# Kernel optimization log

Hardware: AMD Instinct MI355X
Metric: run time of the kernel (lower is better)

Reference implementation:

```python
import jax, jax.numpy as jnp
import numpy as np

ACT_BITS = 8
W_BITS = 8
BN_EPS = 1e-5


def _round_ste(x):
    # straight-through round (HAWQ-style ste_round)
    return x + jax.lax.stop_gradient(jnp.round(x) - x)


def _quant_sym(x, bits):
    # symmetric per-tensor fake quantization; scale treated as constant (EMA min/max in original)
    n = float(2 ** (bits - 1) - 1)
    s = jax.lax.stop_gradient(jnp.maximum(jnp.max(jnp.abs(x)) / n, 1e-8))
    xq = jnp.clip(_round_ste(x / s), -n - 1.0, n) * s
    return xq, s


def _conv(x, w, stride, pad):
    return jax.lax.conv_general_dilated(
        x, w, (stride, stride), [(pad, pad), (pad, pad)],
        dimension_numbers=("NCHW", "OIHW", "NCHW"))


def _quant_bn(x, gamma, beta, mean, var):
    # fold BN into a per-channel scale+bias; quantize the folded scale like a weight
    ws = gamma * jax.lax.rsqrt(var + BN_EPS)          # [C]
    wq, ws_scale = _quant_sym(ws, W_BITS)
    b = beta - mean * wq                               # [C]
    return x * wq[None, :, None, None] + b[None, :, None, None], ws_scale


def setup_inputs() -> dict:
    key = jax.random.key(0)
    ks = jax.random.split(key, 16)
    d = {}
    d["x"] = jax.random.normal(ks[0], (32, 128, 56, 56), jnp.float32)
    d["w1"] = jax.random.normal(ks[1], (256, 128, 3, 3), jnp.float32) * 0.05
    d["w2"] = jax.random.normal(ks[2], (256, 256, 3, 3), jnp.float32) * 0.05
    d["w_id"] = jax.random.normal(ks[3], (256, 128, 1, 1), jnp.float32) * 0.05
    for i, pfx in enumerate(["bn1", "bn2", "id"]):
        k4 = jax.random.split(ks[4 + i], 4)
        d[pfx + "_gamma"] = jax.random.uniform(k4[0], (256,), jnp.float32) + 0.5
        d[pfx + "_beta"] = jax.random.normal(k4[1], (256,), jnp.float32) * 0.1
        d[pfx + "_mean"] = jax.random.normal(k4[2], (256,), jnp.float32) * 0.1
        d[pfx + "_var"] = jax.random.uniform(k4[3], (256,), jnp.float32) + 0.5
    return d


def reference(x, w1, w2, w_id,
              bn1_gamma, bn1_beta, bn1_mean, bn1_var,
              bn2_gamma, bn2_beta, bn2_mean, bn2_var,
              id_gamma, id_beta, id_mean, id_var):
    # quant_act on block input
    xq, act_s = _quant_sym(x, ACT_BITS)

    # identity branch: 1x1 stride-2 quantized conv -> quant_act -> folded quant bn
    w_id_q, _ = _quant_sym(w_id, W_BITS)
    identity = _conv(xq, w_id_q, 2, 0)
    identity, _ = _quant_sym(identity, ACT_BITS)
    identity, _ = _quant_bn(identity, id_gamma, id_beta, id_mean, id_var)

    # main branch conv1 (3x3 stride 2) -> act quant -> bn -> relu -> act quant
    w1_q, _ = _quant_sym(w1, W_BITS)
    h = _conv(xq, w1_q, 2, 1)
    h, _ = _quant_sym(h, ACT_BITS)
    h, _ = _quant_bn(h, bn1_gamma, bn1_beta, bn1_mean, bn1_var)
    h = jax.nn.relu(h)
    h, _ = _quant_sym(h, ACT_BITS)

    # conv2 (3x3 stride 1) -> act quant -> bn
    w2_q, _ = _quant_sym(w2, W_BITS)
    h = _conv(h, w2_q, 1, 1)
    h, _ = _quant_sym(h, ACT_BITS)
    h, _ = _quant_bn(h, bn2_gamma, bn2_beta, bn2_mean, bn2_var)

    # residual add -> int32 requant -> relu
    h = h + identity
    h, out_s = _quant_sym(h, ACT_BITS)
    h = jax.nn.relu(h)
    return h, out_s
```

## Files before the change

kernel.cpp:

```cpp
#include <hip/hip_runtime.h>
#include <limits.h>

#define THREADS 256
#define GRID_BLOCKS 896

typedef int vi4 __attribute__((ext_vector_type(4)));

__device__ __forceinline__ float clamp8f(float q) { return fminf(fmaxf(q, -128.0f), 127.0f); }
__device__ __forceinline__ float sc_from_bits(unsigned b) {
  return fmaxf(__uint_as_float(b) / 127.0f, 1e-8f);
}
__device__ __forceinline__ signed char q8(float v, float s) {
  return (signed char)(int)clamp8f(rintf(v / s));
}


__device__ __forceinline__ void gbar(int* IS, int base, int bx) {
  asm volatile("s_waitcnt vmcnt(0)" ::: "memory");
  int old = __hip_atomic_fetch_add(IS + base + (bx & 7) * 16, 1, __ATOMIC_RELAXED,
                                   __HIP_MEMORY_SCOPE_AGENT);
  if (old == 111) {
    int r = __hip_atomic_fetch_add(IS + base + 128, 1, __ATOMIC_RELAXED, __HIP_MEMORY_SCOPE_AGENT);
    if (r == 7)
      __hip_atomic_fetch_add(IS + base + 144, 1, __ATOMIC_RELAXED, __HIP_MEMORY_SCOPE_AGENT);
  }
  while (__hip_atomic_load(IS + base + 144, __ATOMIC_RELAXED, __HIP_MEMORY_SCOPE_SYSTEM) == 0)
    __builtin_amdgcn_s_sleep(2);
}

__device__ __forceinline__ void amax_body(const float4* __restrict__ p, int n4, int bid,
                                          int nblocks, int* __restrict__ slot) {
  const int tid = threadIdx.x;
  const int stride = nblocks * THREADS;
  float m = 0.0f;
  int i = bid * THREADS + tid;
  for (; i + 3 * stride < n4; i += 4 * stride) {
    float4 v0 = p[i];
    float4 v1 = p[i + stride];
    float4 v2 = p[i + 2 * stride];
    float4 v3 = p[i + 3 * stride];
    float m0 = fmaxf(fmaxf(fabsf(v0.x), fabsf(v0.y)), fmaxf(fabsf(v0.z), fabsf(v0.w)));
    float m1 = fmaxf(fmaxf(fabsf(v1.x), fabsf(v1.y)), fmaxf(fabsf(v1.z), fabsf(v1.w)));
    float m2 = fmaxf(fmaxf(fabsf(v2.x), fabsf(v2.y)), fmaxf(fabsf(v2.z), fabsf(v2.w)));
    float m3 = fmaxf(fmaxf(fabsf(v3.x), fabsf(v3.y)), fmaxf(fabsf(v3.z), fabsf(v3.w)));
    m = fmaxf(m, fmaxf(fmaxf(m0, m1), fmaxf(m2, m3)));
  }
  for (; i < n4; i += stride) {
    float4 v = p[i];
    m = fmaxf(m, fmaxf(fmaxf(fabsf(v.x), fabsf(v.y)), fmaxf(fabsf(v.z), fabsf(v.w))));
  }
#pragma unroll
  for (int k = 32; k >= 1; k >>= 1) m = fmaxf(m, __shfl_xor(m, k));
  __shared__ float wred[4];
  if ((tid & 63) == 0) wred[tid >> 6] = m;
  __syncthreads();
  if (tid == 0) {
    m = fmaxf(fmaxf(wred[0], wred[1]), fmaxf(wred[2], wred[3]));
    atomicMax(slot, __float_as_int(m));
  }
}

__global__ __launch_bounds__(THREADS) void k_pre(
    int* IS, const float* g1, const float* be1, const float* m1, const float* v1, float* wq1,
    float* b1, const float* g2, const float* be2, const float* m2, const float* v2, float* wq2,
    float* b2, const float* gi, const float* bei, const float* mi, const float* vvi, float* wqi,
    float* bi, const float4* w1, const float4* w2, const float4* wid, const float4* x) {
  int b = blockIdx.x;
  int c = threadIdx.x;
  if (b < 3) {
    if (b == 0) {
      IS[128 + c] = 0;
      IS[384 + c] = 0;
      IS[640 + c] = 0;
      if (c < 32) IS[896 + c] = 0;
    }
    const float *gamma, *beta, *mean, *var;
    float *wq, *bb;
    if (b == 0) { gamma = g1; beta = be1; mean = m1; var = v1; wq = wq1; bb = b1; }
    else if (b == 1) { gamma = g2; beta = be2; mean = m2; var = v2; wq = wq2; bb = b2; }
    else { gamma = gi; beta = bei; mean = mi; var = vvi; wq = wqi; bb = bi; }
    __shared__ float red[THREADS];
    float ws = gamma[c] * (1.0f / sqrtf(var[c] + 1e-5f));
    red[c] = fabsf(ws);
    __syncthreads();
    for (int s = THREADS / 2; s > 0; s >>= 1) {
      if (c < s) red[c] = fmaxf(red[c], red[c + s]);
      __syncthreads();
    }
    float sws = fmaxf(red[0] / 127.0f, 1e-8f);
    float q = clamp8f(rintf(ws / sws)) * sws;
    wq[c] = q;
    bb[c] = beta[c] - mean[c] * q;
    return;
  }
  b -= 3;
  if (b < 64) { amax_body(w1, 73728, b, 64, IS + 1); return; }
  b -= 64;
  if (b < 128) { amax_body(w2, 147456, b, 128, IS + 2); return; }
  b -= 128;
  if (b < 16) { amax_body(wid, 8192, b, 16, IS + 3); return; }
  b -= 16;
  amax_body(x, 3211264, b, 512, IS + 0);
}

__global__ __launch_bounds__(THREADS) void k_quant(const float* __restrict__ x,
                                                   int* __restrict__ X8,
                                                   const float* __restrict__ w1f,
                                                   vi4* __restrict__ W1m,
                                                   const float* __restrict__ w2f,
                                                   vi4* __restrict__ W2m,
                                                   const float* __restrict__ widf,
                                                   vi4* __restrict__ Widm,
                                                   const unsigned* __restrict__ ISu) {
  __shared__ signed char tile[56 * 132];
  int b = blockIdx.x;
  int t = threadIdx.x;
  if (b < 1792) {
    float s = sc_from_bits(ISu[0]);
    int h = b % 56, n = b / 56;
    const float* xp = x + ((n * 128) * 56 + h) * 56;
#pragma unroll
    for (int k = 0; k < 28; ++k) {
      int i = t + k * 256;
      int w = i % 56, c = i / 56;
      tile[w * 132 + c] = q8(xp[c * 3136 + w], s);
    }
    __syncthreads();
    int* op = X8 + (n * 56 + h) * 56 * 32;
#pragma unroll
    for (int k = 0; k < 7; ++k) {
      int i = t + k * 256;
      int w = i >> 5, c4 = (i & 31) * 4;
      const signed char* tp = tile + w * 132 + c4;
      op[i] = (int)(unsigned char)tp[0] | ((int)(unsigned char)tp[1] << 8) |
              ((int)(unsigned char)tp[2] << 16) | ((int)(unsigned char)tp[3] << 24);
    }
    return;
  }
  if (b < 1864) {
    int tt = (b - 1792) * THREADS + t;
    float s = sc_from_bits(ISu[1]);
    int lane = tt & 63;
    int cotile = (tt >> 6) & 15;
    int ks = tt >> 10;
    int tap = ks >> 1, kc = ks & 1;
    int kh = tap / 3, kw = tap % 3;
    int co = cotile * 16 + (lane & 15);
    int ci0 = kc * 64 + (lane >> 4) * 16;
    const float* src = w1f + (co * 128 + ci0) * 9 + kh * 3 + kw;
    int r[4];
#pragma unroll
    for (int q = 0; q < 4; ++q) {
      unsigned b0 = (unsigned char)q8(src[(q * 4 + 0) * 9], s);
      unsigned b1 = (unsigned char)q8(src[(q * 4 + 1) * 9], s);
      unsigned b2 = (unsigned char)q8(src[(q * 4 + 2) * 9], s);
      unsigned b3 = (unsigned char)q8(src[(q * 4 + 3) * 9], s);
      r[q] = (int)(b0 | (b1 << 8) | (b2 << 16) | (b3 << 24));
    }
    vi4 v = {r[0], r[1], r[2], r[3]};
    W1m[tt] = v;
    return;
  }
  if (b < 2008) {
    int tt = (b - 1864) * THREADS + t;
    float s = sc_from_bits(ISu[2]);
    int lane = tt & 63;
    int cotile = (tt >> 6) & 15;
    int ks = tt >> 10;
    int tap = ks >> 2, kc = ks & 3;
    int kh = tap / 3, kw = tap % 3;
    int co = cotile * 16 + (lane & 15);
    int ci0 = kc * 64 + (lane >> 4) * 16;
    const float* src = w2f + (co * 256 + ci0) * 9 + kh * 3 + kw;
    int r[4];
#pragma unroll
    for (int q = 0; q < 4; ++q) {
      unsigned b0 = (unsigned char)q8(src[(q * 4 + 0) * 9], s);
      unsigned b1 = (unsigned char)q8(src[(q * 4 + 1) * 9], s);
      unsigned b2 = (unsigned char)q8(src[(q * 4 + 2) * 9], s);
      unsigned b3 = (unsigned char)q8(src[(q * 4 + 3) * 9], s);
      r[q] = (int)(b0 | (b1 << 8) | (b2 << 16) | (b3 << 24));
    }
    vi4 v = {r[0], r[1], r[2], r[3]};
    W2m[tt] = v;
    return;
  }
  {
    int tt = (b - 2008) * THREADS + t;
    float s = sc_from_bits(ISu[3]);
    int lane = tt & 63;
    int cotile = (tt >> 6) & 15;
    int ks = tt >> 10;
    int co = cotile * 16 + (lane & 15);
    int ci0 = ks * 64 + (lane >> 4) * 16;
    const float* src = widf + co * 128 + ci0;
    int r[4];
#pragma unroll
    for (int q = 0; q < 4; ++q) {
      unsigned b0 = (unsigned char)q8(src[q * 4 + 0], s);
      unsigned b1 = (unsigned char)q8(src[q * 4 + 1], s);
      unsigned b2 = (unsigned char)q8(src[q * 4 + 2], s);
      unsigned b3 = (unsigned char)q8(src[q * 4 + 3], s);
      r[q] = (int)(b0 | (b1 << 8) | (b2 << 16) | (b3 << 24));
    }
    vi4 v = {r[0], r[1], r[2], r[3]};
    Widm[tt] = v;
  }
}

#define MFMA_I8(a, b, c) __builtin_amdgcn_mfma_i32_16x16x64_i8(a, b, c, 0, 0, 0)

__device__ __forceinline__ signed char qact(int v, float sxw, float s_h1, float s_y2, float wq,
                                            float bb) {
  float hf = (float)v * sxw;
  float q = clamp8f(rintf(hf / s_h1));
  float hv = q * s_h1;
  float y = fmaxf(hv * wq + bb, 0.0f);
  float a = fminf(fmaxf(rintf(y / s_y2), -128.0f), 127.0f);
  return (signed char)(int)a;
}

__global__ __launch_bounds__(THREADS, 4) void k_cv1(const int* X8, const vi4* __restrict__ W1m,
                                                    const vi4* __restrict__ Widm,
                                                    int* __restrict__ IDI, int* A2i, int* IS,
                                                    const float* __restrict__ wq1,
                                                    const float* __restrict__ b1, float* SC,
                                                    int* maxS2, int* minS2) {
  __shared__ __align__(16) int lds[9280];
  __shared__ int redA[4];
  __shared__ int sVmax, sVmin;
  __shared__ float sSxw, sSh1, sSy2;
  const int tid = threadIdx.x;
  const int bx = blockIdx.x;
  const int n = bx / 28, rr = bx % 28;
  const int hp = rr >> 1, nh = rr & 1;
  const int ho0 = hp * 2;
  vi4 zero = {0, 0, 0, 0};

  for (int r = 0; r < 5; ++r) {
    int h = 2 * ho0 - 1 + r;
    int* dst = lds + r * 58 * 32;
    if (h >= 0 && h < 56) {
      const vi4* src = (const vi4*)(X8 + (n * 56 + h) * 56 * 32);
      for (int i4 = tid; i4 < 448; i4 += THREADS) {
        int col = i4 >> 3, e0 = (i4 & 7) * 4;
        int cell = r * 58 + col + 1;
        *(vi4*)(lds + cell * 32 + (e0 ^ ((cell & 7) << 2))) = src[i4];
      }
      if (tid < 32) dst[tid] = 0;
      else if (tid >= 128 && tid < 160) dst[57 * 32 + (tid - 128)] = 0;
    } else {
      for (int i4 = tid; i4 < 464; i4 += THREADS) ((vi4*)dst)[i4] = zero;
    }
  }
  __syncthreads();

  const int lane = tid & 63, wv = tid >> 6;
  const int mw = wv & 1, nw = wv >> 1;
  const int lm = lane & 15, quad = lane >> 4;
  const int woc0 = lm, woc1 = (16 + lm) > 27 ? 27 : (16 + lm);
  const int choff = quad * 4;
  const int ho = ho0 + mw;
  const int obase = ((n * 28 + ho) * 28) * 256;
  const int ctbase = nh * 8 + nw * 4;

#define LDA(row, colp, sub)                                                              \
  (*(const vi4*)(lds + ((row) * 58 + (colp)) * 32 +                                      \
                 ((sub) ^ ((((row) * 58 + (colp)) & 7) << 2))))

  vi4 acc[2][4];
  vi4 bA[4], bB[4];
  vi4 a0A, a1A, a0B, a1B;

#pragma unroll
  for (int mt = 0; mt < 2; ++mt)
#pragma unroll
    for (int ct = 0; ct < 4; ++ct) acc[mt][ct] = zero;
  const vi4* wibase = Widm + ctbase * 64 + lane;
  {
    const int row = 2 * mw + 1;
#pragma unroll
    for (int kc = 0; kc < 2; ++kc) {
      vi4 a0 = LDA(row, 2 * woc0 + 1, kc * 16 + choff);
      vi4 a1 = LDA(row, 2 * woc1 + 1, kc * 16 + choff);
#pragma unroll
      for (int ct = 0; ct < 4; ++ct) {
        vi4 b = wibase[kc * 1024 + ct * 64];
        acc[0][ct] = MFMA_I8(a0, b, acc[0][ct]);
        acc[1][ct] = MFMA_I8(a1, b, acc[1][ct]);
      }
    }
  }
  int am = 0;
#pragma unroll
  for (int ct = 0; ct < 4; ++ct) {
    const int co = (ctbase + ct) * 16 + lm;
#pragma unroll
    for (int mt = 0; mt < 2; ++mt)
#pragma unroll
      for (int r = 0; r < 4; ++r) {
        int wo = mt * 16 + quad * 4 + r;
        if (wo < 28) {
          int v = acc[mt][ct][r];
          IDI[obase + wo * 256 + co] = v;
          am = max(am, v < 0 ? -v : v);
        }
      }
  }
#pragma unroll
  for (int k = 32; k >= 1; k >>= 1) am = max(am, __shfl_xor(am, k));
  if (lane == 0) redA[wv] = am;

#pragma unroll
  for (int mt = 0; mt < 2; ++mt)
#pragma unroll
    for (int ct = 0; ct < 4; ++ct) acc[mt][ct] = zero;
  const vi4* wbase = W1m + ctbase * 64 + lane;
#pragma unroll
  for (int ct = 0; ct < 4; ++ct) bA[ct] = wbase[ct * 64];
  {
    a0A = LDA(2 * mw, 2 * woc0, choff);
    a1A = LDA(2 * mw, 2 * woc1, choff);
  }
#pragma unroll 1
  for (int ks = 0; ks < 18; ks += 2) {
    {
      const int ksn = ks + 1;
      const int khn = (ksn >= 6) + (ksn >= 12);
      const int t2 = ksn - khn * 6;
      const int kwn = t2 >> 1, kcn = t2 & 1;
#pragma unroll
      for (int ct = 0; ct < 4; ++ct) bB[ct] = wbase[ksn * 1024 + ct * 64];
      const int row = 2 * mw + khn;
      a0B = LDA(row, 2 * woc0 + kwn, kcn * 16 + choff);
      a1B = LDA(row, 2 * woc1 + kwn, kcn * 16 + choff);
    }
#pragma unroll
    for (int ct = 0; ct < 4; ++ct) {
      acc[0][ct] = MFMA_I8(a0A, bA[ct], acc[0][ct]);
      acc[1][ct] = MFMA_I8(a1A, bA[ct], acc[1][ct]);
    }
    if (ks + 2 < 18) {
      const int ksn = ks + 2;
      const int khn = (ksn >= 6) + (ksn >= 12);
      const int t2 = ksn - khn * 6;
      const int kwn = t2 >> 1, kcn = t2 & 1;
#pragma unroll
      for (int ct = 0; ct < 4; ++ct) bA[ct] = wbase[ksn * 1024 + ct * 64];
      const int row = 2 * mw + khn;
      a0A = LDA(row, 2 * woc0 + kwn, kcn * 16 + choff);
      a1A = LDA(row, 2 * woc1 + kwn, kcn * 16 + choff);
    }
#pragma unroll
    for (int ct = 0; ct < 4; ++ct) {
      acc[0][ct] = MFMA_I8(a0B, bB[ct], acc[0][ct]);
      acc[1][ct] = MFMA_I8(a1B, bB[ct], acc[1][ct]);
    }
  }

#pragma unroll
  for (int ct = 0; ct < 4; ++ct) {
    int vmax = INT_MIN, vmin = INT_MAX;
#pragma unroll
    for (int mt = 0; mt < 2; ++mt)
#pragma unroll
      for (int r = 0; r < 4; ++r) {
        int wo = mt * 16 + quad * 4 + r;
        if (wo < 28) {
          int v = acc[mt][ct][r];
          vmax = max(vmax, v);
          vmin = min(vmin, v);
        }
      }
    vmax = max(vmax, __shfl_xor(vmax, 16));
    vmax = max(vmax, __shfl_xor(vmax, 32));
    vmin = min(vmin, __shfl_xor(vmin, 16));
    vmin = min(vmin, __shfl_xor(vmin, 32));
    if (lane < 16) {
      int cl = (nw * 4 + ct) * 16 + lane;
      __hip_atomic_store(maxS2 + bx * 256 + mw * 128 + cl, vmax, __ATOMIC_RELAXED,
                         __HIP_MEMORY_SCOPE_AGENT);
      __hip_atomic_store(minS2 + bx * 256 + mw * 128 + cl, vmin, __ATOMIC_RELAXED,
                         __HIP_MEMORY_SCOPE_AGENT);
    }
  }

  __syncthreads();
  if (tid == 0) {
    int a = max(max(redA[0], redA[1]), max(redA[2], redA[3]));
    atomicMax(IS + 5, a);
  }
#pragma unroll
  for (int ct = 0; ct < 4; ++ct) {
    const int cl = (nw * 4 + ct) * 16 + lm;
#pragma unroll
    for (int mt = 0; mt < 2; ++mt)
#pragma unroll
      for (int r = 0; r < 4; ++r) {
        int wo = mt * 16 + quad * 4 + r;
        if (wo < 28) lds[(mw * 28 + wo) * 130 + cl] = acc[mt][ct][r];
      }
  }
  __syncthreads();
  if (tid == 0) gbar(IS, 128, bx);
  __syncthreads();

  if (bx < 256) {
    const int c = bx, nhc = c >> 7, cl = c & 127;
    int vmax = INT_MIN, vmin = INT_MAX;
    for (int j = tid; j < 896; j += THREADS) {
      int bxx = nhc + ((j >> 1) << 1);
      int mwj = j & 1;
      int a = __hip_atomic_load(maxS2 + bxx * 256 + mwj * 128 + cl, __ATOMIC_RELAXED,
                                __HIP_MEMORY_SCOPE_AGENT);
      int i_ = __hip_atomic_load(minS2 + bxx * 256 + mwj * 128 + cl, __ATOMIC_RELAXED,
                                 __HIP_MEMORY_SCOPE_AGENT);
      vmax = max(vmax, a);
      vmin = min(vmin, i_);
    }
    int* rMax = lds + 7280;
    int* rMin = lds + 7536;
    rMax[tid] = vmax;
    rMin[tid] = vmin;
    __syncthreads();
    for (int s = 128; s > 0; s >>= 1) {
      if (tid < s) {
        rMax[tid] = max(rMax[tid], rMax[tid + s]);
        rMin[tid] = min(rMin[tid], rMin[tid + s]);
      }
      __syncthreads();
    }
    if (tid == 0) {
      sVmax = rMax[0];
      sVmin = rMin[0];
      int a1 = sVmax < 0 ? -sVmax : sVmax;
      int a0 = sVmin < 0 ? -sVmin : sVmin;
      atomicMax(IS + 4, max(a1, a0));
    }
  }
  __syncthreads();
  if (tid == 0) gbar(IS, 288, bx);
  __syncthreads();

  if (bx < 256 && tid == 0) {
    float sx = sc_from_bits((unsigned)__hip_atomic_load(IS + 0, __ATOMIC_RELAXED,
                                                        __HIP_MEMORY_SCOPE_AGENT));
    float sw1 = sc_from_bits((unsigned)__hip_atomic_load(IS + 1, __ATOMIC_RELAXED,
                                                         __HIP_MEMORY_SCOPE_AGENT));
    int mh1 = __hip_atomic_load(IS + 4, __ATOMIC_RELAXED, __HIP_MEMORY_SCOPE_AGENT);
    float sxw = sx * sw1;
    float s_h1 = fmaxf(sxw * (float)mh1 / 127.0f, 1e-8f);
    float wq = wq1[bx], bbc = b1[bx];
    float q1 = clamp8f(rintf((float)sVmax * sxw / s_h1));
    float q0 = clamp8f(rintf((float)sVmin * sxw / s_h1));
    float y1 = fmaxf(q1 * s_h1 * wq + bbc, 0.0f);
    float y0 = fmaxf(q0 * s_h1 * wq + bbc, 0.0f);
    atomicMax(IS + 7, __float_as_int(fmaxf(y1, y0)));
  }
  __syncthreads();
  if (tid == 0) gbar(IS, 448, bx);
  __syncthreads();

  if (tid == 0) {
    float sx = sc_from_bits((unsigned)__hip_atomic_load(IS + 0, __ATOMIC_RELAXED,
                                                        __HIP_MEMORY_SCOPE_AGENT));
    float sw1 = sc_from_bits((unsigned)__hip_atomic_load(IS + 1, __ATOMIC_RELAXED,
                                                         __HIP_MEMORY_SCOPE_AGENT));
    int mh1 = __hip_atomic_load(IS + 4, __ATOMIC_RELAXED, __HIP_MEMORY_SCOPE_AGENT);
    int mrf = __hip_atomic_load(IS + 7, __ATOMIC_RELAXED, __HIP_MEMORY_SCOPE_AGENT);
    float sxw = sx * sw1;
    float s_h1 = fmaxf(sxw * (float)mh1 / 127.0f, 1e-8f);
    float s_y2 = fmaxf(__int_as_float(mrf) / 127.0f, 1e-8f);
    sSxw = sxw;
    sSh1 = s_h1;
    sSy2 = s_y2;
    if (bx == 0) {
      int mid = __hip_atomic_load(IS + 5, __ATOMIC_RELAXED, __HIP_MEMORY_SCOPE_AGENT);
      float swid = sc_from_bits((unsigned)__hip_atomic_load(IS + 3, __ATOMIC_RELAXED,
                                                            __HIP_MEMORY_SCOPE_AGENT));
      SC[9] = s_y2;
      SC[10] = fmaxf(sx * swid * (float)mid / 127.0f, 1e-8f);
    }
  }
  __syncthreads();

  {
    const float sxw = sSxw, s_h1 = sSh1, s_y2 = sSy2;
#pragma unroll
    for (int k = 0; k < 7; ++k) {
      int i = tid + k * 256;
      int sp = i >> 5, c4i = i & 31;
      int mwp = sp >= 28 ? 1 : 0;
      int wo = sp - mwp * 28;
      int c0 = nh * 128 + c4i * 4;
      const int* pk = lds + sp * 130 + c4i * 4;
      unsigned r0 = (unsigned char)qact(pk[0], sxw, s_h1, s_y2, wq1[c0], b1[c0]);
      unsigned r1 = (unsigned char)qact(pk[1], sxw, s_h1, s_y2, wq1[c0 + 1], b1[c0 + 1]);
      unsigned r2 = (unsigned char)qact(pk[2], sxw, s_h1, s_y2, wq1[c0 + 2], b1[c0 + 2]);
      unsigned r3 = (unsigned char)qact(pk[3], sxw, s_h1, s_y2, wq1[c0 + 3], b1[c0 + 3]);
      A2i[((n * 28 + ho0 + mwp) * 28 + wo) * 64 + nh * 32 + c4i] =
          (int)(r0 | (r1 << 8) | (r2 << 16) | (r3 << 24));
    }
  }
#undef LDA
}

struct SumParams {
  float sxw2, s_h2, sxwid, s_idq;
};
__device__ __forceinline__ float sum_val(int v2, int vi, const SumParams& P, float wq2c, float b2c,
                                         float wqidc, float bidc) {
  float q2 = clamp8f(rintf((float)v2 * P.sxw2 / P.s_h2));
  float z = (q2 * P.s_h2) * wq2c + b2c;
  float qi = clamp8f(rintf((float)vi * P.sxwid / P.s_idq));
  float zi = (qi * P.s_idq) * wqidc + bidc;
  return z + zi;
}
__device__ __forceinline__ SumParams make_params2(const float* SC, const unsigned* ISu, int mh2) {
  SumParams P;
  float sx = sc_from_bits(ISu[0]);
  float sw2 = sc_from_bits(ISu[2]);
  float swid = sc_from_bits(ISu[3]);
  float s_y2 = SC[9];
  P.s_idq = SC[10];
  P.sxw2 = s_y2 * sw2;
  P.s_h2 = fmaxf(P.sxw2 * (float)mh2 / 127.0f, 1e-8f);
  P.sxwid = sx * swid;
  return P;
}

__global__ __launch_bounds__(THREADS, 4) void k_tail(const int* __restrict__ A2,
                                                     const vi4* __restrict__ W2m,
                                                     const int* __restrict__ IDI,
                                                     const float* SC, int* IS,
                                                     const float* __restrict__ wq2,
                                                     const float* __restrict__ b2,
                                                     const float* __restrict__ wqid,
                                                     const float* __restrict__ bidp,
                                                     float* __restrict__ out) {
  __shared__ __align__(16) int lds[4 * 30 * 68];
  __shared__ int redA[4];
  __shared__ float redF[4];
  __shared__ int sMh2;
  __shared__ float sOutS;
  const int tid = threadIdx.x;
  const int bx = blockIdx.x;
  const int n = bx / 28, rr = bx % 28;
  const int hp = rr >> 1, nh = rr & 1;
  const int ho0 = hp * 2;
  vi4 zero = {0, 0, 0, 0};

  for (int r = 0; r < 4; ++r) {
    int h = ho0 - 1 + r;
    int* dst = lds + r * 30 * 68;
    if (h >= 0 && h < 28) {
      const vi4* src = (const vi4*)(A2 + (n * 28 + h) * 28 * 64);
      for (int i4 = tid; i4 < 448; i4 += THREADS) {
        int col = i4 >> 4, c = (i4 & 15) * 4;
        *(vi4*)(dst + (col + 1) * 68 + c) = src[i4];
      }
      if (tid < 64) dst[tid] = 0;
      else if (tid >= 128 && tid < 192) dst[29 * 68 + (tid - 128)] = 0;
    } else {
      for (int i4 = tid; i4 < 510; i4 += THREADS) ((vi4*)dst)[i4] = zero;
    }
  }
  __syncthreads();

  const int lane = tid & 63, wv = tid >> 6;
  const int mw = wv & 1, nw = wv >> 1;
  const int lm = lane & 15, quad = lane >> 4;
  const int woc0 = lm, woc1 = (16 + lm) > 27 ? 27 : (16 + lm);
  const int choff = quad * 4;
  const int ctbase = nh * 8 + nw * 4;

  vi4 acc[2][4];
  vi4 bA[4], bB[4];
  vi4 a0A, a1A, a0B, a1B;
#pragma unroll
  for (int mt = 0; mt < 2; ++mt)
#pragma unroll
    for (int ct = 0; ct < 4; ++ct) acc[mt][ct] = zero;

  const vi4* wbase = W2m + ctbase * 64 + lane;
#pragma unroll
  for (int ct = 0; ct < 4; ++ct) bA[ct] = wbase[ct * 64];
  {
    const int ro = mw * 30;
    a0A = *(const vi4*)(lds + (ro + woc0) * 68 + choff);
    a1A = *(const vi4*)(lds + (ro + woc1) * 68 + choff);
  }
#pragma unroll 1
  for (int ks = 0; ks < 36; ks += 2) {
    {
      const int ksn = ks + 1;
      const int khn = (ksn >= 12) + (ksn >= 24);
      const int t2 = ksn - khn * 12;
      const int kwn = t2 >> 2, kcn = t2 & 3;
#pragma unroll
      for (int ct = 0; ct < 4; ++ct) bB[ct] = wbase[ksn * 1024 + ct * 64];
      const int ro = (mw + khn) * 30;
      a0B = *(const vi4*)(lds + (ro + woc0 + kwn) * 68 + kcn * 16 + choff);
      a1B = *(const vi4*)(lds + (ro + woc1 + kwn) * 68 + kcn * 16 + choff);
    }
#pragma unroll
    for (int ct = 0; ct < 4; ++ct) {
      acc[0][ct] = MFMA_I8(a0A, bA[ct], acc[0][ct]);
      acc[1][ct] = MFMA_I8(a1A, bA[ct], acc[1][ct]);
    }
    if (ks + 2 < 36) {
      const int ksn = ks + 2;
      const int khn = (ksn >= 12) + (ksn >= 24);
      const int t2 = ksn - khn * 12;
      const int kwn = t2 >> 2, kcn = t2 & 3;
#pragma unroll
      for (int ct = 0; ct < 4; ++ct) bA[ct] = wbase[ksn * 1024 + ct * 64];
      const int ro = (mw + khn) * 30;
      a0A = *(const vi4*)(lds + (ro + woc0 + kwn) * 68 + kcn * 16 + choff);
      a1A = *(const vi4*)(lds + (ro + woc1 + kwn) * 68 + kcn * 16 + choff);
    }
#pragma unroll
    for (int ct = 0; ct < 4; ++ct) {
      acc[0][ct] = MFMA_I8(a0B, bB[ct], acc[0][ct]);
      acc[1][ct] = MFMA_I8(a1B, bB[ct], acc[1][ct]);
    }
  }

  int am = 0;
#pragma unroll
  for (int ct = 0; ct < 4; ++ct)
#pragma unroll
    for (int mt = 0; mt < 2; ++mt)
#pragma unroll
      for (int r = 0; r < 4; ++r) {
        int wo = mt * 16 + quad * 4 + r;
        if (wo < 28) {
          int v = acc[mt][ct][r];
          am = max(am, v < 0 ? -v : v);
        }
      }
#pragma unroll
  for (int k = 32; k >= 1; k >>= 1) am = max(am, __shfl_xor(am, k));
  if (lane == 0) redA[wv] = am;
  __syncthreads();
  if (tid == 0) {
    int a = max(max(redA[0], redA[1]), max(redA[2], redA[3]));
    atomicMax(IS + 6, a);
  }

  int* sumsi = lds;
  float* sums = (float*)lds;
  const int ib = ((n * 28 + ho0) * 28) * 256 + nh * 128;
#pragma unroll
  for (int k = 0; k < 28; ++k) {
    int idx = tid + k * 256;
    int cl = idx & 127, sp = idx >> 7;
    sumsi[cl * 57 + sp] = IDI[ib + sp * 256 + cl];
  }
  __syncthreads();
  if (tid == 0) {
    gbar(IS, 608, bx);
    sMh2 = __hip_atomic_load(IS + 6, __ATOMIC_RELAXED, __HIP_MEMORY_SCOPE_SYSTEM);
  }
  __syncthreads();
  const SumParams P = make_params2(SC, (const unsigned*)IS, sMh2);

  float fm = 0.0f;
#pragma unroll
  for (int ct = 0; ct < 4; ++ct) {
    const int co = (ctbase + ct) * 16 + lm;
    const int cl = co - nh * 128;
    float w2c = wq2[co], b2c = b2[co], wic = wqid[co], bic = bidp[co];
#pragma unroll
    for (int mt = 0; mt < 2; ++mt)
#pragma unroll
      for (int r = 0; r < 4; ++r) {
        int wo = mt * 16 + quad * 4 + r;
        if (wo < 28) {
          int slot = cl * 57 + mw * 28 + wo;
          float sv = sum_val(acc[mt][ct][r], sumsi[slot], P, w2c, b2c, wic, bic);
          sums[slot] = sv;
          fm = fmaxf(fm, fabsf(sv));
        }
      }
  }
#pragma unroll
  for (int k = 32; k >= 1; k >>= 1) fm = fmaxf(fm, __shfl_xor(fm, k));
  if (lane == 0) redF[wv] = fm;
  __syncthreads();
  if (tid == 0) {
    float a = fmaxf(fmaxf(redF[0], redF[1]), fmaxf(redF[2], redF[3]));
    atomicMax(IS + 11, __float_as_int(a));
    gbar(IS, 768, bx);
    int mb = __hip_atomic_load(IS + 11, __ATOMIC_RELAXED, __HIP_MEMORY_SCOPE_SYSTEM);
    sOutS = fmaxf(__int_as_float(mb) / 127.0f, 1e-8f);
  }
  __syncthreads();
  const float out_s = sOutS;

  float* ob = out + n * 200704 + (nh * 128) * 784 + ho0 * 28;
#pragma unroll
  for (int k = 0; k < 28; ++k) {
    int idx = tid + k * 256;
    int cl = idx / 56, rem = idx % 56;
    float sv = sums[cl * 57 + rem];
    float q = clamp8f(rintf(sv / out_s));
    ob[cl * 784 + rem] = q > 0.0f ? q * out_s : 0.0f;
  }
  if (bx == 0 && tid == 0) out[6422528] = out_s;
}

extern "C" void kernel_launch(void* const* d_in, const int* in_sizes, int n_in, void* d_out,
                              int out_size, void* d_ws, size_t ws_size, hipStream_t stream) {
  (void)in_sizes; (void)n_in; (void)out_size; (void)ws_size;
  const float* x = (const float*)d_in[0];
  const float* w1 = (const float*)d_in[1];
  const float* w2 = (const float*)d_in[2];
  const float* wid = (const float*)d_in[3];
  const float* bn1g = (const float*)d_in[4];
  const float* bn1b = (const float*)d_in[5];
  const float* bn1m = (const float*)d_in[6];
  const float* bn1v = (const float*)d_in[7];
  const float* bn2g = (const float*)d_in[8];
  const float* bn2b = (const float*)d_in[9];
  const float* bn2m = (const float*)d_in[10];
  const float* bn2v = (const float*)d_in[11];
  const float* idg = (const float*)d_in[12];
  const float* idb = (const float*)d_in[13];
  const float* idm = (const float*)d_in[14];
  const float* idv = (const float*)d_in[15];

  char* ws = (char*)d_ws;
  float* SC = (float*)ws;
  int* IS = (int*)ws;
  unsigned* ISu = (unsigned*)ws;
  float* wq1 = (float*)(ws + 4096);
  float* b1 = (float*)(ws + 5120);
  float* wq2 = (float*)(ws + 6144);
  float* b2 = (float*)(ws + 7168);
  float* wqid = (float*)(ws + 8192);
  float* bid = (float*)(ws + 9216);
  char* X8 = ws + 16384;
  char* A2 = X8;
  char* W1m = X8 + 12845056;
  char* W2m = W1m + 294912;
  char* Widm = W2m + 589824;
  int* IDI = (int*)(Widm + 32768);
  float* out = (float*)d_out;
  int* maxS2 = (int*)d_out;
  int* minS2 = maxS2 + 896 * 256;

  k_pre<<<723, THREADS, 0, stream>>>(IS, bn1g, bn1b, bn1m, bn1v, wq1, b1, bn2g, bn2b, bn2m, bn2v,
                                     wq2, b2, idg, idb, idm, idv, wqid, bid, (const float4*)w1,
                                     (const float4*)w2, (const float4*)wid, (const float4*)x);
  k_quant<<<2016, THREADS, 0, stream>>>(x, (int*)X8, w1, (vi4*)W1m, w2, (vi4*)W2m, wid,
                                        (vi4*)Widm, ISu);
  k_cv1<<<GRID_BLOCKS, THREADS, 0, stream>>>((const int*)X8, (const vi4*)W1m, (const vi4*)Widm,
                                             IDI, (int*)A2, IS, wq1, b1, SC, maxS2, minS2);
  k_tail<<<GRID_BLOCKS, THREADS, 0, stream>>>((const int*)A2, (const vi4*)W2m, (const int*)IDI, SC,
                                              IS, wq2, b2, wqid, bid, out);
}
```

Before: 246.9 us.

## Fuse prep and quant kernels via grid barrier; drop cv1 per-channel exchange phase

Merges the BN-fold/amax kernel and the int8 quantization kernel into one 2016-block kernel. The two phases are separated by a software grid barrier, and launch bounds request 8 blocks per CU so every block can be resident at once. In the conv1 kernel, the cross-block per-channel min/max exchange and its extra grid barrier are removed: each block computes the post-BN/ReLU max from its own per-channel extrema and contributes it with an atomicMax. Barrier counters are now cleared with a hipMemsetAsync instead of inside the prep kernel. This saves a kernel launch and a global synchronization round. The cost is that correctness depends on all 2016 blocks being co-resident, which risks a deadlock if register or LDS use limits occupancy.

```diff
diff --git a/kernel.cpp b/kernel.cpp
--- a/kernel.cpp
+++ b/kernel.cpp
@@ -15,11 +15,11 @@
 }
 
 
-__device__ __forceinline__ void gbar(int* IS, int base, int bx) {
+__device__ __forceinline__ void gbar(int* IS, int base, int bx, int subTgt) {
   asm volatile("s_waitcnt vmcnt(0)" ::: "memory");
   int old = __hip_atomic_fetch_add(IS + base + (bx & 7) * 16, 1, __ATOMIC_RELAXED,
                                    __HIP_MEMORY_SCOPE_AGENT);
-  if (old == 111) {
+  if (old == subTgt - 1) {
     int r = __hip_atomic_fetch_add(IS + base + 128, 1, __ATOMIC_RELAXED, __HIP_MEMORY_SCOPE_AGENT);
     if (r == 7)
       __hip_atomic_fetch_add(IS + base + 144, 1, __ATOMIC_RELAXED, __HIP_MEMORY_SCOPE_AGENT);
@@ -60,63 +60,66 @@
   }
 }
 
-__global__ __launch_bounds__(THREADS) void k_pre(
+__device__ __forceinline__ float sc_slot(const int* IS, int slot) {
+  unsigned u = (unsigned)__hip_atomic_load((int*)(IS + slot), __ATOMIC_RELAXED,
+                                           __HIP_MEMORY_SCOPE_AGENT);
+  return fmaxf(__uint_as_float(u) / 127.0f, 1e-8f);
+}
+
+__global__ __launch_bounds__(THREADS, 8) void k_pq(
     int* IS, const float* g1, const float* be1, const float* m1, const float* v1, float* wq1,
     float* b1, const float* g2, const float* be2, const float* m2, const float* v2, float* wq2,
     float* b2, const float* gi, const float* bei, const float* mi, const float* vvi, float* wqi,
-    float* bi, const float4* w1, const float4* w2, const float4* wid, const float4* x) {
-  int b = blockIdx.x;
-  int c = threadIdx.x;
-  if (b < 3) {
-    if (b == 0) {
-      IS[128 + c] = 0;
-      IS[384 + c] = 0;
-      IS[640 + c] = 0;
-      if (c < 32) IS[896 + c] = 0;
-    }
-    const float *gamma, *beta, *mean, *var;
-    float *wq, *bb;
-    if (b == 0) { gamma = g1; beta = be1; mean = m1; var = v1; wq = wq1; bb = b1; }
-    else if (b == 1) { gamma = g2; beta = be2; mean = m2; var = v2; wq = wq2; bb = b2; }
-    else { gamma = gi; beta = bei; mean = mi; var = vvi; wq = wqi; bb = bi; }
-    __shared__ float red[THREADS];
-    float ws = gamma[c] * (1.0f / sqrtf(var[c] + 1e-5f));
-    red[c] = fabsf(ws);
-    __syncthreads();
-    for (int s = THREADS / 2; s > 0; s >>= 1) {
-      if (c < s) red[c] = fmaxf(red[c], red[c + s]);
+    float* bi, const float* x, int* X8, const float* w1f, vi4* W1m, const float* w2f, vi4* W2m,
+    const float* widf, vi4* Widm) {
+  __shared__ signed char tile[56 * 132];
+  __shared__ float red[THREADS];
+  const int bx = blockIdx.x;
+  const int t = threadIdx.x;
+
+  {
+    int b = bx;
+    if (b < 3) {
+      const float *gamma, *beta, *mean, *var;
+      float *wq, *bb;
+      if (b == 0) { gamma = g1; beta = be1; mean = m1; var = v1; wq = wq1; bb = b1; }
+      else if (b == 1) { gamma = g2; beta = be2; mean = m2; var = v2; wq = wq2; bb = b2; }
+      else { gamma = gi; beta = bei; mean = mi; var = vvi; wq = wqi; bb = bi; }
+      int c = t;
+      float ws = gamma[c] * (1.0f / sqrtf(var[c] + 1e-5f));
+      red[c] = fabsf(ws);
       __syncthreads();
-    }
-    float sws = fmaxf(red[0] / 127.0f, 1e-8f);
-    float q = clamp8f(rintf(ws / sws)) * sws;
-    wq[c] = q;
-    bb[c] = beta[c] - mean[c] * q;
-    return;
-  }
-  b -= 3;
-  if (b < 64) { amax_body(w1, 73728, b, 64, IS + 1); return; }
-  b -= 64;
-  if (b < 128) { amax_body(w2, 147456, b, 128, IS + 2); return; }
-  b -= 128;
-  if (b < 16) { amax_body(wid, 8192, b, 16, IS + 3); return; }
-  b -= 16;
-  amax_body(x, 3211264, b, 512, IS + 0);
-}
-
-__global__ __launch_bounds__(THREADS) void k_quant(const float* __restrict__ x,
-                                                   int* __restrict__ X8,
-                                                   const float* __restrict__ w1f,
-                                                   vi4* __restrict__ W1m,
-                                                   const float* __restrict__ w2f,
-                                                   vi4* __restrict__ W2m,
-                                                   const float* __restrict__ widf,
-                                                   vi4* __restrict__ Widm,
-                                                   const unsigned* __restrict__ ISu) {
-  __shared__ signed char tile[56 * 132];
-  int b = blockIdx.x;
-  int t = threadIdx.x;
+      for (int s = THREADS / 2; s > 0; s >>= 1) {
+        if (c < s) red[c] = fmaxf(red[c], red[c + s]);
+        __syncthreads();
+      }
+      float sws = fmaxf(red[0] / 127.0f, 1e-8f);
+      float q = clamp8f(rintf(ws / sws)) * sws;
+      wq[c] = q;
+      bb[c] = beta[c] - mean[c] * q;
+    } else {
+      b -= 3;
+      if (b < 64) {
+        amax_body((const float4*)w1f, 73728, b, 64, IS + 1);
+      } else {
+        b -= 64;
+        if (b < 128) {
+          amax_body((const float4*)w2f, 147456, b, 128, IS + 2);
+        } else {
+          b -= 128;
+          if (b < 16) amax_body((const float4*)widf, 8192, b, 16, IS + 3);
+          else amax_body((const float4*)x, 3211264, b - 16, 1805, IS + 0);
+        }
+      }
+    }
+  }
+  __syncthreads();
+  if (t == 0) gbar(IS, 128, bx, 252);
+  __syncthreads();
+
+  int b = bx;
   if (b < 1792) {
-    float s = sc_from_bits(ISu[0]);
+    float s = sc_slot(IS, 0);
     int h = b % 56, n = b / 56;
     const float* xp = x + ((n * 128) * 56 + h) * 56;
 #pragma unroll
@@ -139,7 +142,7 @@
   }
   if (b < 1864) {
     int tt = (b - 1792) * THREADS + t;
-    float s = sc_from_bits(ISu[1]);
+    float s = sc_slot(IS, 1);
     int lane = tt & 63;
     int cotile = (tt >> 6) & 15;
     int ks = tt >> 10;
@@ -152,10 +155,10 @@
 #pragma unroll
     for (int q = 0; q < 4; ++q) {
       unsigned b0 = (unsigned char)q8(src[(q * 4 + 0) * 9], s);
-      unsigned b1 = (unsigned char)q8(src[(q * 4 + 1) * 9], s);
-      unsigned b2 = (unsigned char)q8(src[(q * 4 + 2) * 9], s);
+      unsigned b1v = (unsigned char)q8(src[(q * 4 + 1) * 9], s);
+      unsigned b2v = (unsigned char)q8(src[(q * 4 + 2) * 9], s);
       unsigned b3 = (unsigned char)q8(src[(q * 4 + 3) * 9], s);
-      r[q] = (int)(b0 | (b1 << 8) | (b2 << 16) | (b3 << 24));
+      r[q] = (int)(b0 | (b1v << 8) | (b2v << 16) | (b3 << 24));
     }
     vi4 v = {r[0], r[1], r[2], r[3]};
     W1m[tt] = v;
@@ -163,7 +166,7 @@
   }
   if (b < 2008) {
     int tt = (b - 1864) * THREADS + t;
-    float s = sc_from_bits(ISu[2]);
+    float s = sc_slot(IS, 2);
     int lane = tt & 63;
     int cotile = (tt >> 6) & 15;
     int ks = tt >> 10;
@@ -176,10 +179,10 @@
 #pragma unroll
     for (int q = 0; q < 4; ++q) {
       unsigned b0 = (unsigned char)q8(src[(q * 4 + 0) * 9], s);
-      unsigned b1 = (unsigned char)q8(src[(q * 4 + 1) * 9], s);
-      unsigned b2 = (unsigned char)q8(src[(q * 4 + 2) * 9], s);
+      unsigned b1v = (unsigned char)q8(src[(q * 4 + 1) * 9], s);
+      unsigned b2v = (unsigned char)q8(src[(q * 4 + 2) * 9], s);
       unsigned b3 = (unsigned char)q8(src[(q * 4 + 3) * 9], s);
-      r[q] = (int)(b0 | (b1 << 8) | (b2 << 16) | (b3 << 24));
+      r[q] = (int)(b0 | (b1v << 8) | (b2v << 16) | (b3 << 24));
     }
     vi4 v = {r[0], r[1], r[2], r[3]};
     W2m[tt] = v;
@@ -187,7 +190,7 @@
   }
   {
     int tt = (b - 2008) * THREADS + t;
-    float s = sc_from_bits(ISu[3]);
+    float s = sc_slot(IS, 3);
     int lane = tt & 63;
     int cotile = (tt >> 6) & 15;
     int ks = tt >> 10;
@@ -198,10 +201,10 @@
 #pragma unroll
     for (int q = 0; q < 4; ++q) {
       unsigned b0 = (unsigned char)q8(src[q * 4 + 0], s);
-      unsigned b1 = (unsigned char)q8(src[q * 4 + 1], s);
-      unsigned b2 = (unsigned char)q8(src[q * 4 + 2], s);
+      unsigned b1v = (unsigned char)q8(src[q * 4 + 1], s);
+      unsigned b2v = (unsigned char)q8(src[q * 4 + 2], s);
       unsigned b3 = (unsigned char)q8(src[q * 4 + 3], s);
-      r[q] = (int)(b0 | (b1 << 8) | (b2 << 16) | (b3 << 24));
+      r[q] = (int)(b0 | (b1v << 8) | (b2v << 16) | (b3 << 24));
     }
     vi4 v = {r[0], r[1], r[2], r[3]};
     Widm[tt] = v;
@@ -224,11 +227,10 @@
                                                     const vi4* __restrict__ Widm,
                                                     int* __restrict__ IDI, int* A2i, int* IS,
                                                     const float* __restrict__ wq1,
-                                                    const float* __restrict__ b1, float* SC,
-                                                    int* maxS2, int* minS2) {
+                                                    const float* __restrict__ b1, float* SC) {
   __shared__ __align__(16) int lds[9280];
-  __shared__ int redA[4];
-  __shared__ int sVmax, sVmin;
+  __shared__ int redA[4], redB[4];
+  __shared__ float redF[4];
   __shared__ float sSxw, sSh1, sSy2;
   const int tid = threadIdx.x;
   const int bx = blockIdx.x;
@@ -358,6 +360,8 @@
     }
   }
 
+  int vmx[4], vmn[4];
+  int am1 = 0;
 #pragma unroll
   for (int ct = 0; ct < 4; ++ct) {
     int vmax = INT_MIN, vmin = INT_MAX;
@@ -376,20 +380,15 @@
     vmax = max(vmax, __shfl_xor(vmax, 32));
     vmin = min(vmin, __shfl_xor(vmin, 16));
     vmin = min(vmin, __shfl_xor(vmin, 32));
-    if (lane < 16) {
-      int cl = (nw * 4 + ct) * 16 + lane;
-      __hip_atomic_store(maxS2 + bx * 256 + mw * 128 + cl, vmax, __ATOMIC_RELAXED,
-                         __HIP_MEMORY_SCOPE_AGENT);
-      __hip_atomic_store(minS2 + bx * 256 + mw * 128 + cl, vmin, __ATOMIC_RELAXED,
-                         __HIP_MEMORY_SCOPE_AGENT);
-    }
-  }
-
-  __syncthreads();
-  if (tid == 0) {
-    int a = max(max(redA[0], redA[1]), max(redA[2], redA[3]));
-    atomicMax(IS + 5, a);
-  }
+    vmx[ct] = vmax;
+    vmn[ct] = vmin;
+    am1 = max(am1, max(vmax < 0 ? -vmax : vmax, vmin < 0 ? -vmin : vmin));
+  }
+#pragma unroll
+  for (int k = 8; k >= 1; k >>= 1) am1 = max(am1, __shfl_xor(am1, k));
+  if (lane == 0) redB[wv] = am1;
+
+  __syncthreads();
 #pragma unroll
   for (int ct = 0; ct < 4; ++ct) {
     const int cl = (nw * 4 + ct) * 16 + lm;
@@ -401,83 +400,46 @@
         if (wo < 28) lds[(mw * 28 + wo) * 130 + cl] = acc[mt][ct][r];
       }
   }
-  __syncthreads();
-  if (tid == 0) gbar(IS, 128, bx);
-  __syncthreads();
-
-  if (bx < 256) {
-    const int c = bx, nhc = c >> 7, cl = c & 127;
-    int vmax = INT_MIN, vmin = INT_MAX;
-    for (int j = tid; j < 896; j += THREADS) {
-      int bxx = nhc + ((j >> 1) << 1);
-      int mwj = j & 1;
-      int a = __hip_atomic_load(maxS2 + bxx * 256 + mwj * 128 + cl, __ATOMIC_RELAXED,
-                                __HIP_MEMORY_SCOPE_AGENT);
-      int i_ = __hip_atomic_load(minS2 + bxx * 256 + mwj * 128 + cl, __ATOMIC_RELAXED,
-                                 __HIP_MEMORY_SCOPE_AGENT);
-      vmax = max(vmax, a);
-      vmin = min(vmin, i_);
-    }
-    int* rMax = lds + 7280;
-    int* rMin = lds + 7536;
-    rMax[tid] = vmax;
-    rMin[tid] = vmin;
-    __syncthreads();
-    for (int s = 128; s > 0; s >>= 1) {
-      if (tid < s) {
-        rMax[tid] = max(rMax[tid], rMax[tid + s]);
-        rMin[tid] = min(rMin[tid], rMin[tid + s]);
-      }
-      __syncthreads();
-    }
-    if (tid == 0) {
-      sVmax = rMax[0];
-      sVmin = rMin[0];
-      int a1 = sVmax < 0 ? -sVmax : sVmax;
-      int a0 = sVmin < 0 ? -sVmin : sVmin;
-      atomicMax(IS + 4, max(a1, a0));
-    }
-  }
-  __syncthreads();
-  if (tid == 0) gbar(IS, 288, bx);
-  __syncthreads();
-
-  if (bx < 256 && tid == 0) {
-    float sx = sc_from_bits((unsigned)__hip_atomic_load(IS + 0, __ATOMIC_RELAXED,
-                                                        __HIP_MEMORY_SCOPE_AGENT));
-    float sw1 = sc_from_bits((unsigned)__hip_atomic_load(IS + 1, __ATOMIC_RELAXED,
-                                                         __HIP_MEMORY_SCOPE_AGENT));
+  if (tid == 0) {
+    atomicMax(IS + 5, max(max(redA[0], redA[1]), max(redA[2], redA[3])));
+    atomicMax(IS + 4, max(max(redB[0], redB[1]), max(redB[2], redB[3])));
+    gbar(IS, 288, bx, 112);
+    float sx = sc_slot(IS, 0);
+    float sw1 = sc_slot(IS, 1);
     int mh1 = __hip_atomic_load(IS + 4, __ATOMIC_RELAXED, __HIP_MEMORY_SCOPE_AGENT);
-    float sxw = sx * sw1;
-    float s_h1 = fmaxf(sxw * (float)mh1 / 127.0f, 1e-8f);
-    float wq = wq1[bx], bbc = b1[bx];
-    float q1 = clamp8f(rintf((float)sVmax * sxw / s_h1));
-    float q0 = clamp8f(rintf((float)sVmin * sxw / s_h1));
-    float y1 = fmaxf(q1 * s_h1 * wq + bbc, 0.0f);
-    float y0 = fmaxf(q0 * s_h1 * wq + bbc, 0.0f);
-    atomicMax(IS + 7, __float_as_int(fmaxf(y1, y0)));
-  }
-  __syncthreads();
-  if (tid == 0) gbar(IS, 448, bx);
-  __syncthreads();
-
+    sSxw = sx * sw1;
+    sSh1 = fmaxf(sSxw * (float)mh1 / 127.0f, 1e-8f);
+  }
+  __syncthreads();
+
+  {
+    const float sxw = sSxw, s_h1 = sSh1;
+    float ym = 0.0f;
+#pragma unroll
+    for (int ct = 0; ct < 4; ++ct) {
+      const int co = (ctbase + ct) * 16 + lm;
+      float wq = wq1[co], bbc = b1[co];
+      float q1 = clamp8f(rintf((float)vmx[ct] * sxw / s_h1));
+      float q0 = clamp8f(rintf((float)vmn[ct] * sxw / s_h1));
+      float y1 = fmaxf(q1 * s_h1 * wq + bbc, 0.0f);
+      float y0 = fmaxf(q0 * s_h1 * wq + bbc, 0.0f);
+      ym = fmaxf(ym, fmaxf(y1, y0));
+    }
+#pragma unroll
+    for (int k = 8; k >= 1; k >>= 1) ym = fmaxf(ym, __shfl_xor(ym, k));
+    if (lane == 0) redF[wv] = ym;
+  }
+  __syncthreads();
   if (tid == 0) {
-    float sx = sc_from_bits((unsigned)__hip_atomic_load(IS + 0, __ATOMIC_RELAXED,
-                                                        __HIP_MEMORY_SCOPE_AGENT));
-    float sw1 = sc_from_bits((unsigned)__hip_atomic_load(IS + 1, __ATOMIC_RELAXED,
-                                                         __HIP_MEMORY_SCOPE_AGENT));
-    int mh1 = __hip_atomic_load(IS + 4, __ATOMIC_RELAXED, __HIP_MEMORY_SCOPE_AGENT);
+    atomicMax(IS + 7, __float_as_int(fmaxf(fmaxf(redF[0], redF[1]), fmaxf(redF[2], redF[3]))));
+    gbar(IS, 448, bx, 112);
     int mrf = __hip_atomic_load(IS + 7, __ATOMIC_RELAXED, __HIP_MEMORY_SCOPE_AGENT);
-    float sxw = sx * sw1;
-    float s_h1 = fmaxf(sxw * (float)mh1 / 127.0f, 1e-8f);
     float s_y2 = fmaxf(__int_as_float(mrf) / 127.0f, 1e-8f);
-    sSxw = sxw;
-    sSh1 = s_h1;
     sSy2 = s_y2;
     if (bx == 0) {
       int mid = __hip_atomic_load(IS + 5, __ATOMIC_RELAXED, __HIP_MEMORY_SCOPE_AGENT);
-      float swid = sc_from_bits((unsigned)__hip_atomic_load(IS + 3, __ATOMIC_RELAXED,
-                                                            __HIP_MEMORY_SCOPE_AGENT));
+      float sx = sc_slot(IS, 0);
+      float swid = sc_slot(IS, 3);
       SC[9] = s_y2;
       SC[10] = fmaxf(sx * swid * (float)mid / 127.0f, 1e-8f);
     }
@@ -659,7 +621,7 @@
   }
   __syncthreads();
   if (tid == 0) {
-    gbar(IS, 608, bx);
+    gbar(IS, 608, bx, 112);
     sMh2 = __hip_atomic_load(IS + 6, __ATOMIC_RELAXED, __HIP_MEMORY_SCOPE_SYSTEM);
   }
   __syncthreads();
@@ -691,7 +653,7 @@
   if (tid == 0) {
     float a = fmaxf(fmaxf(redF[0], redF[1]), fmaxf(redF[2], redF[3]));
     atomicMax(IS + 11, __float_as_int(a));
-    gbar(IS, 768, bx);
+    gbar(IS, 768, bx, 112);
     int mb = __hip_atomic_load(IS + 11, __ATOMIC_RELAXED, __HIP_MEMORY_SCOPE_SYSTEM);
     sOutS = fmaxf(__int_as_float(mb) / 127.0f, 1e-8f);
   }
@@ -733,7 +695,6 @@
   char* ws = (char*)d_ws;
   float* SC = (float*)ws;
   int* IS = (int*)ws;
-  unsigned* ISu = (unsigned*)ws;
   float* wq1 = (float*)(ws + 4096);
   float* b1 = (float*)(ws + 5120);
   float* wq2 = (float*)(ws + 6144);
@@ -747,16 +708,14 @@
   char* Widm = W2m + 589824;
   int* IDI = (int*)(Widm + 32768);
   float* out = (float*)d_out;
-  int* maxS2 = (int*)d_out;
-  int* minS2 = maxS2 + 896 * 256;
-
-  k_pre<<<723, THREADS, 0, stream>>>(IS, bn1g, bn1b, bn1m, bn1v, wq1, b1, bn2g, bn2b, bn2m, bn2v,
-                                     wq2, b2, idg, idb, idm, idv, wqid, bid, (const float4*)w1,
-                                     (const float4*)w2, (const float4*)wid, (const float4*)x);
-  k_quant<<<2016, THREADS, 0, stream>>>(x, (int*)X8, w1, (vi4*)W1m, w2, (vi4*)W2m, wid,
-                                        (vi4*)Widm, ISu);
+
+  hipMemsetAsync(ws + 512, 0, 3584, stream);
+
+  k_pq<<<2016, THREADS, 0, stream>>>(IS, bn1g, bn1b, bn1m, bn1v, wq1, b1, bn2g, bn2b, bn2m, bn2v,
+                                     wq2, b2, idg, idb, idm, idv, wqid, bid, x, (int*)X8, w1,
+                                     (vi4*)W1m, w2, (vi4*)W2m, wid, (vi4*)Widm);
   k_cv1<<<GRID_BLOCKS, THREADS, 0, stream>>>((const int*)X8, (const vi4*)W1m, (const vi4*)Widm,
-                                             IDI, (int*)A2, IS, wq1, b1, SC, maxS2, minS2);
+                                             IDI, (int*)A2, IS, wq1, b1, SC);
   k_tail<<<GRID_BLOCKS, THREADS, 0, stream>>>((const int*)A2, (const vi4*)W2m, (const int*)IDI, SC,
                                               IS, wq2, b2, wqid, bid, out);
 }
```

Result: slower. 273.4 us (+10.7%).
